# Kernel tuning notes

Measured on AMD Instinct MI355X. Metric: run time of the kernel, lower is better.

## Reference

```python
import jax, jax.numpy as jnp
import numpy as np

N_A, N_B = 50000, 10000
E = 300000
IN_F, HID, BEL_OUT, INC_OUT = 256, 256, 128, 128


def _gconv(x_src, W, b, src, dst, n_src, n_dst):
    """DGL GraphConv with norm='both': D_in^{-1/2} A D_out^{-1/2} X W + b, degs clamped to >=1."""
    ones = jnp.ones(src.shape[0], x_src.dtype)
    deg_out = jnp.maximum(jax.ops.segment_sum(ones, src, num_segments=n_src), 1.0)
    deg_in = jnp.maximum(jax.ops.segment_sum(ones, dst, num_segments=n_dst), 1.0)
    h = (x_src * jax.lax.rsqrt(deg_out)[:, None]) @ W        # [n_src, out]
    agg = jax.ops.segment_sum(h[src], dst, num_segments=n_dst)  # scatter-add messages
    return agg * jax.lax.rsqrt(deg_in)[:, None] + b


def setup_inputs() -> dict:
    key = jax.random.key(0)
    ks = jax.random.split(key, 12)
    s = 1.0 / np.sqrt(IN_F)
    sh = 1.0 / np.sqrt(HID)
    return {
        "x_a": jax.random.normal(ks[0], (N_A, IN_F), jnp.float32),
        "x_b": jax.random.normal(ks[1], (N_B, IN_F), jnp.float32),
        "W1_bel": jax.random.normal(ks[2], (IN_F, HID), jnp.float32) * s,
        "b1_bel": jnp.zeros((HID,), jnp.float32),
        "W1_inc": jax.random.normal(ks[3], (IN_F, HID), jnp.float32) * s,
        "b1_inc": jnp.zeros((HID,), jnp.float32),
        "W2_bel": jax.random.normal(ks[4], (HID, BEL_OUT), jnp.float32) * sh,
        "b2_bel": jnp.zeros((BEL_OUT,), jnp.float32),
        "W2_inc": jax.random.normal(ks[5], (HID, INC_OUT), jnp.float32) * sh,
        "b2_inc": jnp.zeros((INC_OUT,), jnp.float32),
        "bel_src": jax.random.randint(ks[6], (E,), 0, N_A, jnp.int32),
        "bel_dst": jax.random.randint(ks[7], (E,), 0, N_B, jnp.int32),
        "inc_src": jax.random.randint(ks[8], (E,), 0, N_B, jnp.int32),
        "inc_dst": jax.random.randint(ks[9], (E,), 0, N_A, jnp.int32),
    }


def reference(x_a, x_b, W1_bel, b1_bel, W1_inc, b1_inc, W2_bel, b2_bel,
              W2_inc, b2_inc, bel_src, bel_dst, inc_src, inc_dst):
    n_a, n_b = x_a.shape[0], x_b.shape[0]
    # layer 1 (HeteroGraphConv, mean over a single relation per dst type = identity)
    h_b = _gconv(x_a, W1_bel, b1_bel, bel_src, bel_dst, n_a, n_b)  # 'belongs_to': A->B
    h_a = _gconv(x_b, W1_inc, b1_inc, inc_src, inc_dst, n_b, n_a)  # 'including' : B->A
    h_a = jax.nn.relu(h_a)
    h_b = jax.nn.relu(h_b)
    # layer 2
    out_b = _gconv(h_a, W2_bel, b2_bel, bel_src, bel_dst, n_a, n_b)  # [N_B, bel_out]
    out_a = _gconv(h_b, W2_inc, b2_inc, inc_src, inc_dst, n_b, n_a)  # [N_A, inc_out]
    return out_a, out_b
```

## Files before the change

### kernel.cpp

```cpp
#include <hip/hip_runtime.h>


#define NA 50000
#define NB 10000
#define NE 300000
#define GB 625
#define HB 1172
#define PB 64
#define CB 300

typedef unsigned short u16;
typedef unsigned int u32;
typedef __attribute__((ext_vector_type(8))) short short8;
typedef __attribute__((ext_vector_type(4))) float f32x4;
typedef __attribute__((ext_vector_type(2))) float f32x2;
typedef __attribute__((ext_vector_type(4))) unsigned short u16x4;
typedef __attribute__((ext_vector_type(4))) int i32x4;

__device__ __forceinline__ int xcc_id(){
  return (int)(__builtin_amdgcn_s_getreg(63508) & 7u);
}

__device__ __forceinline__ float bf2f(u16 h){
  union { u32 u; float f; } x; x.u = ((u32)h) << 16; return x.f;
}
__device__ __forceinline__ u16 f2bf(float f){
  union { float f; u32 u; } x; x.f = f;
  u32 r = (x.u + 0x7FFFu + ((x.u >> 16) & 1u)) >> 16;
  return (u16)r;
}

__device__ __forceinline__ void pack_elem(int t,
    const float* __restrict__ W1b, const float* __restrict__ W1i,
    const float* __restrict__ W2b, const float* __restrict__ W2i,
    u16* __restrict__ pwh, u16* __restrict__ pwl){
  const float* W; int N; int tt;
  if (t < 65536)       { W = W1b; N = 256; tt = t; }
  else if (t < 131072) { W = W1i; N = 256; tt = t - 65536; }
  else if (t < 163840) { W = W2b; N = 128; tt = t - 131072; }
  else                 { W = W2i; N = 128; tt = t - 163840; }
  int j = tt & 7, lane = (tt >> 3) & 63, tile = tt >> 9;
  int nT = N >> 4;
  int nt = tile % nT, kt = tile / nT;
  int k = kt * 32 + ((lane >> 4) << 3) + j;
  int n = nt * 16 + (lane & 15);
  float v = W[k * N + n];
  u16 hi = f2bf(v);
  pwh[t] = hi;
  pwl[t] = f2bf(v - bf2f(hi));
}

__global__ __launch_bounds__(256) void pre_kernel(
    int* __restrict__ z, int nz4, const float* __restrict__ W1i,
    u16* __restrict__ pwh, u16* __restrict__ pwl){
  int g = blockIdx.x * blockDim.x + threadIdx.x;
  int s = gridDim.x * blockDim.x;
  i32x4* z4 = (i32x4*)z;
  i32x4 zero = {0, 0, 0, 0};
  for (int i = g; i < nz4; i += s) __builtin_nontemporal_store(zero, z4 + i);
  for (int t = g; t < 65536; t += s)
    pack_elem(65536 + t, nullptr, W1i, nullptr, nullptr, pwh, pwl);
}

__device__ __forceinline__ void gemm_dev(int blk, const float* __restrict__ A,
                                         const u16* __restrict__ PWH,
                                         const u16* __restrict__ PWL,
                                         const float* __restrict__ bias,
                                         const float* __restrict__ rs,
                                         float* __restrict__ Cf,
                                         u16* __restrict__ C16,
                                         int M, int nT, int wpsShift,
                                         int doRelu, int ldC, int colOff){
  int wave = blk * 4 + (threadIdx.x >> 6);
  int lane = threadIdx.x & 63;
  int strips = M >> 4;
  int strip = wave >> wpsShift;
  if (strip >= strips) return;
  int slice = wave & ((1 << wpsShift) - 1);
  int ntPer = nT >> wpsShift;
  int ntStart = slice * ntPer;
  int r16 = lane & 15, quad = lane >> 4;
  int m0 = strip << 4;
  const float* aBase = A + (size_t)(m0 + r16) * 256 + quad * 8;
  short8 ah[8], al[8];
#pragma unroll
  for (int kt = 0; kt < 8; ++kt){
    float4 p0 = *(const float4*)(aBase + kt * 32);
    float4 p1 = *(const float4*)(aBase + kt * 32 + 4);
    float v[8] = {p0.x, p0.y, p0.z, p0.w, p1.x, p1.y, p1.z, p1.w};
    short8 h, l;
#pragma unroll
    for (int j = 0; j < 8; ++j){
      u16 hb = f2bf(v[j]);
      h[j] = (short)hb;
      l[j] = (short)f2bf(v[j] - bf2f(hb));
    }
    ah[kt] = h; al[kt] = l;
  }
  float rscale[4];
#pragma unroll
  for (int r = 0; r < 4; ++r) rscale[r] = rs ? rs[m0 + quad * 4 + r] : 1.f;
  for (int nt = ntStart; nt < ntStart + ntPer; ++nt){
    f32x4 acc = {0.f, 0.f, 0.f, 0.f};
    const u16* bh = PWH + ((size_t)nt * 64 + lane) * 8;
    const u16* bl = PWL + ((size_t)nt * 64 + lane) * 8;
#pragma unroll
    for (int kt = 0; kt < 8; ++kt){
      short8 wh = *(const short8*)(bh + (size_t)kt * nT * 512);
      short8 wl = *(const short8*)(bl + (size_t)kt * nT * 512);
      acc = __builtin_amdgcn_mfma_f32_16x16x32_bf16(ah[kt], wh, acc, 0, 0, 0);
      acc = __builtin_amdgcn_mfma_f32_16x16x32_bf16(al[kt], wh, acc, 0, 0, 0);
      acc = __builtin_amdgcn_mfma_f32_16x16x32_bf16(ah[kt], wl, acc, 0, 0, 0);
    }
    int col = nt * 16 + r16;
    float bv = bias ? bias[col] : 0.f;
#pragma unroll
    for (int r = 0; r < 4; ++r){
      float v = acc[r] * rscale[r] + bv;
      if (doRelu) v = fmaxf(v, 0.f);
      size_t o = (size_t)(m0 + quad * 4 + r) * ldC + colOff + col;
      if (C16) __builtin_nontemporal_store(f2bf(v), C16 + o);
      else     __builtin_nontemporal_store(v, Cf + o);
    }
  }
}

__global__ __launch_bounds__(256) void mega_kernel(
    const float* __restrict__ xb,
    const u16* __restrict__ WH1i, const u16* __restrict__ WL1i,
    u16* __restrict__ G12,
    const int* __restrict__ bs, const int* __restrict__ bd,
    const int* __restrict__ isc, const int* __restrict__ idt,
    int* __restrict__ c_bs8, int* __restrict__ c_bd8,
    int* __restrict__ c_is8, int* __restrict__ c_id,
    int* __restrict__ rank_bel, int* __restrict__ rank_inc,
    const float* __restrict__ W1b, const float* __restrict__ W2b,
    const float* __restrict__ W2i,
    u16* __restrict__ pwh, u16* __restrict__ pwl,
    const float* __restrict__ xa, u16* __restrict__ xa16){
  int blk = blockIdx.x;
  if (blk < GB){
    gemm_dev(blk, xb, WH1i, WL1i, nullptr, nullptr,
             nullptr, G12, NB, 16, 2, 0, 384, 0);
  } else if (blk < GB + HB){
    int xcc = xcc_id();
    int g = (blk - GB) * blockDim.x + threadIdx.x;
    int s = HB * blockDim.x;
    for (int e = g; e < NE; e += s){
      __hip_atomic_fetch_add(&c_bs8[bs[e] * 8 + xcc], 1,
                             __ATOMIC_RELAXED, __HIP_MEMORY_SCOPE_WORKGROUP);
      int rb = __hip_atomic_fetch_add(&c_bd8[bd[e] * 8 + xcc], 1,
                             __ATOMIC_RELAXED, __HIP_MEMORY_SCOPE_WORKGROUP);
      rank_bel[e] = rb | (xcc << 27);
      __hip_atomic_fetch_add(&c_is8[isc[e] * 8 + xcc], 1,
                             __ATOMIC_RELAXED, __HIP_MEMORY_SCOPE_WORKGROUP);
      rank_inc[e] = atomicAdd(&c_id[idt[e]], 1);
    }
  } else if (blk < GB + HB + PB){
    int g = (blk - GB - HB) * blockDim.x + threadIdx.x;
    int s = PB * blockDim.x;
    for (int v = g; v < 131072; v += s){
      int t = v < 65536 ? v : v + 65536;
      pack_elem(t, W1b, nullptr, W2b, W2i, pwh, pwl);
    }
  } else {
    int g = ((blk - GB - HB - PB) * blockDim.x + threadIdx.x) * 4;
    int s = CB * blockDim.x * 4;
    for (int i = g; i < NA * 256; i += s){
      float4 v = *(const float4*)(xa + i);
      u16x4 o;
      o.x = f2bf(v.x); o.y = f2bf(v.y); o.z = f2bf(v.z); o.w = f2bf(v.w);
      __builtin_nontemporal_store(o, (u16x4*)(xa16 + i));
    }
  }
}

__global__ __launch_bounds__(1024) void scan_scales_kernel(
    const int* __restrict__ c_bs8, const int* __restrict__ c_bd8,
    const int* __restrict__ c_is8, const int* __restrict__ c_id,
    int* __restrict__ off_bel, int* __restrict__ off_inc,
    float* __restrict__ s_ob, float* __restrict__ s_ib,
    float* __restrict__ s_oi, float* __restrict__ s_ii){
  if (blockIdx.x >= 2){
    int g = (blockIdx.x - 2) * blockDim.x + threadIdx.x;
    int s = (gridDim.x - 2) * blockDim.x;
    for (int i = g; i < NA; i += s){
      i32x4 a0 = *(const i32x4*)(c_bs8 + i * 8);
      i32x4 a1 = *(const i32x4*)(c_bs8 + i * 8 + 4);
      int a = a0[0] + a0[1] + a0[2] + a0[3] + a1[0] + a1[1] + a1[2] + a1[3];
      s_ob[i] = rsqrtf((float)(a > 1 ? a : 1));
      int b = c_id[i]; s_ii[i] = rsqrtf((float)(b > 1 ? b : 1));
      if (i < NB){
        i32x4 c0 = *(const i32x4*)(c_bd8 + i * 8);
        i32x4 c1 = *(const i32x4*)(c_bd8 + i * 8 + 4);
        int c = c0[0] + c0[1] + c0[2] + c0[3] + c1[0] + c1[1] + c1[2] + c1[3];
        s_ib[i] = rsqrtf((float)(c > 1 ? c : 1));
        i32x4 d0 = *(const i32x4*)(c_is8 + i * 8);
        i32x4 d1 = *(const i32x4*)(c_is8 + i * 8 + 4);
        int d = d0[0] + d0[1] + d0[2] + d0[3] + d1[0] + d1[1] + d1[2] + d1[3];
        s_oi[i] = rsqrtf((float)(d > 1 ? d : 1));
      }
    }
    return;
  }
  __shared__ int wsum[16];
  int tid = threadIdx.x, lane = tid & 63, wid = tid >> 6;
  if (blockIdx.x == 0){
    const int SEG = 10;
    int i0 = tid * SEG;
    int v[SEG];
#pragma unroll
    for (int r = 0; r < SEG; ++r){
      int idx = i0 + r;
      int sv = 0;
      if (idx < NB){
        i32x4 q0 = *(const i32x4*)(c_bd8 + idx * 8);
        i32x4 q1 = *(const i32x4*)(c_bd8 + idx * 8 + 4);
        sv = q0[0] + q0[1] + q0[2] + q0[3] + q1[0] + q1[1] + q1[2] + q1[3];
      }
      v[r] = sv;
    }
    int sum = 0;
#pragma unroll
    for (int r = 0; r < SEG; ++r) sum += v[r];
    int x = sum;
#pragma unroll
    for (int d = 1; d < 64; d <<= 1){
      int t = __shfl_up(x, d, 64);
      if (lane >= d) x += t;
    }
    if (lane == 63) wsum[wid] = x;
    __syncthreads();
    if (wid == 0){
      int ws = (lane < 16) ? wsum[lane] : 0;
#pragma unroll
      for (int d = 1; d < 16; d <<= 1){
        int t = __shfl_up(ws, d, 64);
        if (lane >= d) ws += t;
      }
      if (lane < 16) wsum[lane] = ws;
    }
    __syncthreads();
    int run = (wid ? wsum[wid - 1] : 0) + (x - sum);
#pragma unroll
    for (int r = 0; r < SEG; ++r){
      int idx = i0 + r;
      if (idx < NB) off_bel[idx] = run;
      run += v[r];
    }
    if (tid == 0) off_bel[NB] = wsum[15];
  } else {
    const int n = NA;
    int seg = (n + 1023) >> 10;
    int i0 = tid * seg;
    int lim = i0 + seg; if (lim > n) lim = n;
    int sum = 0;
    for (int i = i0; i < lim; ++i) sum += c_id[i];
    int x = sum;
#pragma unroll
    for (int d = 1; d < 64; d <<= 1){
      int t = __shfl_up(x, d, 64);
      if (lane >= d) x += t;
    }
    if (lane == 63) wsum[wid] = x;
    __syncthreads();
    if (wid == 0){
      int ws = (lane < 16) ? wsum[lane] : 0;
#pragma unroll
      for (int d = 1; d < 16; d <<= 1){
        int t = __shfl_up(ws, d, 64);
        if (lane >= d) ws += t;
      }
      if (lane < 16) wsum[lane] = ws;
    }
    __syncthreads();
    int run = (wid ? wsum[wid - 1] : 0) + (x - sum);
    for (int i = i0; i < lim; ++i){ off_inc[i] = run; run += c_id[i]; }
    if (tid == 0) off_inc[n] = wsum[15];
  }
}

__global__ __launch_bounds__(256) void fill_kernel(
    const int* __restrict__ bs, const int* __restrict__ bd,
    const int* __restrict__ isc, const int* __restrict__ idt,
    const int* __restrict__ rank_bel, const int* __restrict__ rank_inc,
    const int* __restrict__ off_bel, const int* __restrict__ off_inc,
    const int* __restrict__ c_bd8,
    int* __restrict__ csr_bel, int* __restrict__ csr_inc){
  int g = blockIdx.x * blockDim.x + threadIdx.x;
  int s = gridDim.x * blockDim.x;
  for (int e = g; e < NE; e += s){
    int pb = rank_bel[e];
    int xcc = pb >> 27;
    int rb = pb & ((1 << 27) - 1);
    int d = bd[e];
    i32x4 q0 = *(const i32x4*)(c_bd8 + d * 8);
    i32x4 q1 = *(const i32x4*)(c_bd8 + d * 8 + 4);
    int p = 0;
    p += (xcc > 0) ? q0[0] : 0;
    p += (xcc > 1) ? q0[1] : 0;
    p += (xcc > 2) ? q0[2] : 0;
    p += (xcc > 3) ? q0[3] : 0;
    p += (xcc > 4) ? q1[0] : 0;
    p += (xcc > 5) ? q1[1] : 0;
    p += (xcc > 6) ? q1[2] : 0;
    csr_bel[off_bel[d] + p + rb] = bs[e];
    csr_inc[off_inc[idt[e]] + rank_inc[e]] = isc[e];
  }
}

__global__ __launch_bounds__(256) void agg_bel_kernel(
    const u16* __restrict__ X, const float* __restrict__ ss,
    const int* __restrict__ off, const int* __restrict__ csr,
    float* __restrict__ Pf, int nDst){
  int wave = blockIdx.x * 4 + (threadIdx.x >> 6);
  int lane = threadIdx.x & 63;
  if (wave >= nDst) return;
  int b0 = off[wave], b1 = off[wave + 1];
  int deg = b1 - b0;
  int part = lane >> 5;
  int cl = lane & 31;
  int c = cl * 8;
  float acc[8];
#pragma unroll
  for (int q = 0; q < 8; ++q) acc[q] = 0.f;
  int idx = 0; float sc = 0.f;
  if (lane < deg){
    idx = csr[b0 + lane];
    sc = ss ? ss[idx] : 1.f;
  }
  int lim = deg < 64 ? deg : 64;
  for (int u = 0; u < lim; u += 8){
    const u16* addr[4]; float w[4];
#pragma unroll
    for (int k = 0; k < 4; ++k){
      int e = u + k * 2 + part;
      int t = e < lim ? e : 0;
      int s0 = __shfl(idx, t, 64);
      float c0 = __shfl(sc, t, 64);
      w[k] = e < lim ? c0 : 0.f;
      addr[k] = X + (size_t)s0 * 256 + c;
    }
    short8 v[4];
#pragma unroll
    for (int k = 0; k < 4; ++k) v[k] = *(const short8*)addr[k];
#pragma unroll
    for (int k = 0; k < 4; ++k)
#pragma unroll
      for (int q = 0; q < 8; ++q) acc[q] += bf2f((u16)v[k][q]) * w[k];
  }
  for (int j = b0 + 64 + part; j < b1; j += 2){
    int s0 = csr[j];
    float c0 = ss ? ss[s0] : 1.f;
    short8 v0 = *(const short8*)(X + (size_t)s0 * 256 + c);
#pragma unroll
    for (int q = 0; q < 8; ++q) acc[q] += bf2f((u16)v0[q]) * c0;
  }
#pragma unroll
  for (int q = 0; q < 8; ++q) acc[q] += __shfl_xor(acc[q], 32, 64);
  if (part == 0){
    f32x4 f0 = {acc[0], acc[1], acc[2], acc[3]};
    f32x4 f1 = {acc[4], acc[5], acc[6], acc[7]};
    __builtin_nontemporal_store(f0, (f32x4*)(Pf + (size_t)wave * 256 + c));
    __builtin_nontemporal_store(f1, (f32x4*)(Pf + (size_t)wave * 256 + c + 4));
  }
}

__global__ __launch_bounds__(256) void gemmHG_kernel(
    const float* __restrict__ Pb,
    const u16* __restrict__ WH1b, const u16* __restrict__ WL1b,
    const float* __restrict__ b1b, const float* __restrict__ s_ib,
    const u16* __restrict__ WH2i, const u16* __restrict__ WL2i,
    u16* __restrict__ G12){
  __shared__ float Hs[16][260];
  int w = threadIdx.x >> 6;
  int lane = threadIdx.x & 63;
  int r16 = lane & 15, quad = lane >> 4;
  int m0 = blockIdx.x << 4;
  const float* aBase = Pb + (size_t)(m0 + r16) * 256 + quad * 8;
  short8 ah[8], al[8];
#pragma unroll
  for (int kt = 0; kt < 8; ++kt){
    float4 p0 = *(const float4*)(aBase + kt * 32);
    float4 p1 = *(const float4*)(aBase + kt * 32 + 4);
    float v[8] = {p0.x, p0.y, p0.z, p0.w, p1.x, p1.y, p1.z, p1.w};
    short8 h, l;
#pragma unroll
    for (int j = 0; j < 8; ++j){
      u16 hb = f2bf(v[j]);
      h[j] = (short)hb;
      l[j] = (short)f2bf(v[j] - bf2f(hb));
    }
    ah[kt] = h; al[kt] = l;
  }
  float rs1[4];
#pragma unroll
  for (int r = 0; r < 4; ++r) rs1[r] = s_ib[m0 + quad * 4 + r];
  for (int nt = w * 4; nt < w * 4 + 4; ++nt){
    f32x4 acc = {0.f, 0.f, 0.f, 0.f};
    const u16* bh = WH1b + ((size_t)nt * 64 + lane) * 8;
    const u16* bl = WL1b + ((size_t)nt * 64 + lane) * 8;
#pragma unroll
    for (int kt = 0; kt < 8; ++kt){
      short8 wh = *(const short8*)(bh + (size_t)kt * 16 * 512);
      short8 wl = *(const short8*)(bl + (size_t)kt * 16 * 512);
      acc = __builtin_amdgcn_mfma_f32_16x16x32_bf16(ah[kt], wh, acc, 0, 0, 0);
      acc = __builtin_amdgcn_mfma_f32_16x16x32_bf16(al[kt], wh, acc, 0, 0, 0);
      acc = __builtin_amdgcn_mfma_f32_16x16x32_bf16(ah[kt], wl, acc, 0, 0, 0);
    }
    int col = nt * 16 + r16;
    float bv = b1b[col];
#pragma unroll
    for (int r = 0; r < 4; ++r)
      Hs[quad * 4 + r][col] = fmaxf(acc[r] * rs1[r] + bv, 0.f);
  }
  __syncthreads();
  short8 ah2[8], al2[8];
#pragma unroll
  for (int kt = 0; kt < 8; ++kt){
    float4 p0 = *(const float4*)&Hs[r16][kt * 32 + quad * 8];
    float4 p1 = *(const float4*)&Hs[r16][kt * 32 + quad * 8 + 4];
    float v[8] = {p0.x, p0.y, p0.z, p0.w, p1.x, p1.y, p1.z, p1.w};
    short8 h, l;
#pragma unroll
    for (int j = 0; j < 8; ++j){
      u16 hb = f2bf(v[j]);
      h[j] = (short)hb;
      l[j] = (short)f2bf(v[j] - bf2f(hb));
    }
    ah2[kt] = h; al2[kt] = l;
  }
  for (int nt = w * 2; nt < w * 2 + 2; ++nt){
    f32x4 acc = {0.f, 0.f, 0.f, 0.f};
    const u16* bh = WH2i + ((size_t)nt * 64 + lane) * 8;
    const u16* bl = WL2i + ((size_t)nt * 64 + lane) * 8;
#pragma unroll
    for (int kt = 0; kt < 8; ++kt){
      short8 wh = *(const short8*)(bh + (size_t)kt * 8 * 512);
      short8 wl = *(const short8*)(bl + (size_t)kt * 8 * 512);
      acc = __builtin_amdgcn_mfma_f32_16x16x32_bf16(ah2[kt], wh, acc, 0, 0, 0);
      acc = __builtin_amdgcn_mfma_f32_16x16x32_bf16(al2[kt], wh, acc, 0, 0, 0);
      acc = __builtin_amdgcn_mfma_f32_16x16x32_bf16(ah2[kt], wl, acc, 0, 0, 0);
    }
    int col = nt * 16 + r16;
#pragma unroll
    for (int r = 0; r < 4; ++r){
      u16 o = f2bf(acc[r]);
      __builtin_nontemporal_store(o, G12 + (size_t)(m0 + quad * 4 + r) * 384 + 256 + col);
    }
  }
}

__global__ __launch_bounds__(256) void agg_inc2_kernel(
    const u16* __restrict__ G12, const int* __restrict__ off,
    const int* __restrict__ csr, const float* __restrict__ s_oi,
    const float* __restrict__ s_ii, const float* __restrict__ s_ob,
    const float* __restrict__ b1i, const float* __restrict__ b2i,
    u16* __restrict__ Ha, float* __restrict__ outa){
  int wave = blockIdx.x * 4 + (threadIdx.x >> 6);
  int lane = threadIdx.x & 63;
  if (wave >= NA) return;
  int b0 = off[wave], b1 = off[wave + 1];
  int deg = b1 - b0;
  int c1 = lane * 4;
  int c2 = lane * 2;
  float acc[6];
#pragma unroll
  for (int q = 0; q < 6; ++q) acc[q] = 0.f;
  int idx = 0; float sc = 0.f;
  if (lane < deg){
    idx = csr[b0 + lane];
    sc = s_oi[idx];
  }
  int lim = deg < 64 ? deg : 64;
  for (int u = 0; u < lim; u += 4){
    ushort4 va[4]; ushort2 vb[4]; float w[4];
#pragma unroll
    for (int k = 0; k < 4; ++k){
      int e = u + k;
      int t = e < lim ? e : 0;
      int se = __shfl(idx, t, 64);
      float c0 = __shfl(sc, t, 64);
      w[k] = e < lim ? c0 : 0.f;
      const u16* r = G12 + (size_t)se * 384;
      va[k] = *(const ushort4*)(r + c1);
      vb[k] = *(const ushort2*)(r + 256 + c2);
    }
#pragma unroll
    for (int k = 0; k < 4; ++k){
      acc[0] += bf2f(va[k].x) * w[k];
      acc[1] += bf2f(va[k].y) * w[k];
      acc[2] += bf2f(va[k].z) * w[k];
      acc[3] += bf2f(va[k].w) * w[k];
      acc[4] += bf2f(vb[k].x) * w[k];
      acc[5] += bf2f(vb[k].y) * w[k];
    }
  }
  for (int j = b0 + 64; j < b1; ++j){
    int se = csr[j];
    float c0 = s_oi[se];
    const u16* r = G12 + (size_t)se * 384;
    ushort4 va = *(const ushort4*)(r + c1);
    ushort2 vb = *(const ushort2*)(r + 256 + c2);
    acc[0] += bf2f(va.x) * c0; acc[1] += bf2f(va.y) * c0;
    acc[2] += bf2f(va.z) * c0; acc[3] += bf2f(va.w) * c0;
    acc[4] += bf2f(vb.x) * c0; acc[5] += bf2f(vb.y) * c0;
  }
  float sii = s_ii[wave], sob = s_ob[wave];
  float4 bb1 = *(const float4*)(b1i + c1);
  f32x2 bb2 = *(const f32x2*)(b2i + c2);
  u16x4 o1;
  o1.x = f2bf(fmaxf(acc[0] * sii + bb1.x, 0.f) * sob);
  o1.y = f2bf(fmaxf(acc[1] * sii + bb1.y, 0.f) * sob);
  o1.z = f2bf(fmaxf(acc[2] * sii + bb1.z, 0.f) * sob);
  o1.w = f2bf(fmaxf(acc[3] * sii + bb1.w, 0.f) * sob);
  __builtin_nontemporal_store(o1, (u16x4*)(Ha + (size_t)wave * 256 + c1));
  f32x2 o2 = {acc[4] * sii + bb2.x, acc[5] * sii + bb2.y};
  __builtin_nontemporal_store(o2, (f32x2*)(outa + (size_t)wave * 128 + c2));
}

__global__ __launch_bounds__(256) void gemm_kernel(
    const float* __restrict__ A,
    const u16* __restrict__ PWH, const u16* __restrict__ PWL,
    const float* __restrict__ bias, const float* __restrict__ rs,
    float* __restrict__ Cf, u16* __restrict__ C16,
    int M, int nT, int wpsShift, int doRelu, int ldC, int colOff){
  gemm_dev(blockIdx.x, A, PWH, PWL, bias, rs, Cf, C16,
           M, nT, wpsShift, doRelu, ldC, colOff);
}

extern "C" void kernel_launch(void* const* d_in, const int* in_sizes, int n_in,
                              void* d_out, int out_size, void* d_ws, size_t ws_size,
                              hipStream_t stream){
  const float* x_a = (const float*)d_in[0];
  const float* x_b = (const float*)d_in[1];
  const float* W1b = (const float*)d_in[2];
  const float* b1b = (const float*)d_in[3];
  const float* W1i = (const float*)d_in[4];
  const float* b1i = (const float*)d_in[5];
  const float* W2b = (const float*)d_in[6];
  const float* b2b = (const float*)d_in[7];
  const float* W2i = (const float*)d_in[8];
  const float* b2i = (const float*)d_in[9];
  const int* bs  = (const int*)d_in[10];
  const int* bd  = (const int*)d_in[11];
  const int* isc = (const int*)d_in[12];
  const int* idt = (const int*)d_in[13];

  char* w = (char*)d_ws;
  size_t o = 0;
  auto take = [&](size_t bytes) -> void* {
    void* p = w + o; o = (o + bytes + 255) & ~(size_t)255; return p;
  };
  int* zint = (int*)take((size_t)610000 * sizeof(int));
  int* c_bs8 = zint;
  int* c_bd8 = zint + 400000;
  int* c_is8 = zint + 480000;
  int* c_id  = zint + 560000;
  int* rank_bel = (int*)take(NE * sizeof(int));
  int* rank_inc = (int*)take(NE * sizeof(int));
  int* off_bel = (int*)take((NB + 1) * sizeof(int));
  int* off_inc = (int*)take((NA + 1) * sizeof(int));
  int* csr_bel = (int*)take(NE * sizeof(int));
  int* csr_inc = (int*)take(NE * sizeof(int));
  float* s_ob = (float*)take(NA * sizeof(float));
  float* s_ib = (float*)take(NB * sizeof(float));
  float* s_oi = (float*)take(NB * sizeof(float));
  float* s_ii = (float*)take(NA * sizeof(float));
  u16* pwh = (u16*)take(196608 * sizeof(u16));
  u16* pwl = (u16*)take(196608 * sizeof(u16));
  u16* pwh1b = pwh, *pwh1i = pwh + 65536, *pwh2b = pwh + 131072, *pwh2i = pwh + 163840;
  u16* pwl1b = pwl, *pwl1i = pwl + 65536, *pwl2b = pwl + 131072, *pwl2i = pwl + 163840;
  u16* xa16 = (u16*)take((size_t)NA * 256 * sizeof(u16));
  u16* G12  = (u16*)take((size_t)NB * 384 * sizeof(u16));
  u16* H_a  = (u16*)take((size_t)NA * 256 * sizeof(u16));
  float* P_b = (float*)take((size_t)NB * 256 * sizeof(float));

  float* out_a = (float*)d_out;
  float* out_b = (float*)d_out + (size_t)NA * 128;

  pre_kernel<<<256, 256, 0, stream>>>(zint, 610000 / 4, W1i, pwh, pwl);
  mega_kernel<<<GB + HB + PB + CB, 256, 0, stream>>>(
      x_b, pwh1i, pwl1i, G12,
      bs, bd, isc, idt, c_bs8, c_bd8, c_is8, c_id, rank_bel, rank_inc,
      W1b, W2b, W2i, pwh, pwl, x_a, xa16);
  scan_scales_kernel<<<52, 1024, 0, stream>>>(c_bs8, c_bd8, c_is8, c_id,
                                              off_bel, off_inc,
                                              s_ob, s_ib, s_oi, s_ii);
  fill_kernel<<<1172, 256, 0, stream>>>(bs, bd, isc, idt, rank_bel, rank_inc,
                                        off_bel, off_inc, c_bd8,
                                        csr_bel, csr_inc);
  agg_bel_kernel<<<2500, 256, 0, stream>>>(xa16, s_ob, off_bel, csr_bel, P_b, NB);
  gemmHG_kernel<<<625, 256, 0, stream>>>(P_b, pwh1b, pwl1b, b1b, s_ib,
                                         pwh2i, pwl2i, G12);
  agg_inc2_kernel<<<12500, 256, 0, stream>>>(G12, off_inc, csr_inc, s_oi,
                                             s_ii, s_ob, b1i, b2i, H_a, out_a);
  agg_bel_kernel<<<2500, 256, 0, stream>>>(H_a, nullptr, off_bel, csr_bel, P_b, NB);
  gemm_kernel<<<625, 256, 0, stream>>>(P_b, pwh2b, pwl2b, b2b, s_ib,
                                       out_b, nullptr, NB, 8, 2, 0, 128, 0);
}
```

Baseline: 395.2 us.

## Compute source out-degrees via LDS-privatized packed 16-bit histograms per edge slice

Out-degree counts for bel_src and inc_src are now built in pre_kernel, with LDS histograms per edge slice using packed 16-bit counters. Slice partials are written to global memory and reduced in scan_scales_kernel. Destination counters drop the per-XCC 8-way replication and go back to plain global atomics, which simplifies fill_kernel's CSR placement. The aim is to remove two global atomic streams from mega_kernel and shrink the zeroed workspace, at the cost of 64-way partial reductions per node and more contention on the single destination counters.

```diff
diff --git a/kernel.cpp b/kernel.cpp
--- a/kernel.cpp
+++ b/kernel.cpp
@@ -8,6 +8,10 @@
 #define HB 1172
 #define PB 64
 #define CB 300
+#define NSL 64
+#define EPS 4688
+#define NWBS 12500
+#define NWIS 5000
 
 typedef unsigned short u16;
 typedef unsigned int u32;
@@ -16,10 +20,6 @@
 typedef __attribute__((ext_vector_type(2))) float f32x2;
 typedef __attribute__((ext_vector_type(4))) unsigned short u16x4;
 typedef __attribute__((ext_vector_type(4))) int i32x4;
-
-__device__ __forceinline__ int xcc_id(){
-  return (int)(__builtin_amdgcn_s_getreg(63508) & 7u);
-}
 
 __device__ __forceinline__ float bf2f(u16 h){
   union { u32 u; float f; } x; x.u = ((u32)h) << 16; return x.f;
@@ -51,15 +51,46 @@
 }
 
 __global__ __launch_bounds__(256) void pre_kernel(
-    int* __restrict__ z, int nz4, const float* __restrict__ W1i,
+    const int* __restrict__ bs, const int* __restrict__ isc,
+    u32* __restrict__ pbs, u32* __restrict__ pis,
+    int* __restrict__ zint, int nz, const float* __restrict__ W1i,
     u16* __restrict__ pwh, u16* __restrict__ pwl){
-  int g = blockIdx.x * blockDim.x + threadIdx.x;
-  int s = gridDim.x * blockDim.x;
-  i32x4* z4 = (i32x4*)z;
-  i32x4 zero = {0, 0, 0, 0};
-  for (int i = g; i < nz4; i += s) __builtin_nontemporal_store(zero, z4 + i);
-  for (int t = g; t < 65536; t += s)
-    pack_elem(65536 + t, nullptr, W1i, nullptr, nullptr, pwh, pwl);
+  __shared__ u32 lh[NWBS];
+  int blk = blockIdx.x, tid = threadIdx.x;
+  if (blk < 192){
+    int isB = blk >= 128;
+    int slice = isB ? (blk - 128) : (blk & 63);
+    int range = isB ? 0 : (blk >> 6);
+    int nw = isB ? NWIS : NWBS;
+    int lo = range * 25000;
+    int nbins = isB ? NB : 25000;
+    const int* src = isB ? isc : bs;
+    u32* dst = isB ? (pis + (size_t)slice * NWIS)
+                   : (pbs + (size_t)blk * NWBS);
+    for (int i = tid; i < nw; i += 256) lh[i] = 0;
+    __syncthreads();
+    int e0 = slice * EPS;
+    int e1 = e0 + EPS; if (e1 > NE) e1 = NE;
+    const i32x4* s4 = (const i32x4*)src;
+    for (int i = e0 / 4 + tid; i < e1 / 4; i += 256){
+      i32x4 v = s4[i];
+#pragma unroll
+      for (int k = 0; k < 4; ++k){
+        int b = v[k] - lo;
+        if ((unsigned)b < (unsigned)nbins)
+          atomicAdd(&lh[b >> 1], 1u << ((b & 1) << 4));
+      }
+    }
+    __syncthreads();
+    for (int i = tid; i < nw; i += 256)
+      __builtin_nontemporal_store(lh[i], dst + i);
+  } else {
+    int g = (blk - 192) * 256 + tid;
+    int s = 128 * 256;
+    for (int i = g; i < nz; i += s) zint[i] = 0;
+    for (int t = g; t < 65536; t += s)
+      pack_elem(65536 + t, nullptr, W1i, nullptr, nullptr, pwh, pwl);
+  }
 }
 
 __device__ __forceinline__ void gemm_dev(int blk, const float* __restrict__ A,
@@ -129,10 +160,8 @@
     const float* __restrict__ xb,
     const u16* __restrict__ WH1i, const u16* __restrict__ WL1i,
     u16* __restrict__ G12,
-    const int* __restrict__ bs, const int* __restrict__ bd,
-    const int* __restrict__ isc, const int* __restrict__ idt,
-    int* __restrict__ c_bs8, int* __restrict__ c_bd8,
-    int* __restrict__ c_is8, int* __restrict__ c_id,
+    const int* __restrict__ bd, const int* __restrict__ idt,
+    int* __restrict__ c_bd, int* __restrict__ c_id,
     int* __restrict__ rank_bel, int* __restrict__ rank_inc,
     const float* __restrict__ W1b, const float* __restrict__ W2b,
     const float* __restrict__ W2i,
@@ -143,17 +172,10 @@
     gemm_dev(blk, xb, WH1i, WL1i, nullptr, nullptr,
              nullptr, G12, NB, 16, 2, 0, 384, 0);
   } else if (blk < GB + HB){
-    int xcc = xcc_id();
     int g = (blk - GB) * blockDim.x + threadIdx.x;
     int s = HB * blockDim.x;
     for (int e = g; e < NE; e += s){
-      __hip_atomic_fetch_add(&c_bs8[bs[e] * 8 + xcc], 1,
-                             __ATOMIC_RELAXED, __HIP_MEMORY_SCOPE_WORKGROUP);
-      int rb = __hip_atomic_fetch_add(&c_bd8[bd[e] * 8 + xcc], 1,
-                             __ATOMIC_RELAXED, __HIP_MEMORY_SCOPE_WORKGROUP);
-      rank_bel[e] = rb | (xcc << 27);
-      __hip_atomic_fetch_add(&c_is8[isc[e] * 8 + xcc], 1,
-                             __ATOMIC_RELAXED, __HIP_MEMORY_SCOPE_WORKGROUP);
+      rank_bel[e] = atomicAdd(&c_bd[bd[e]], 1);
       rank_inc[e] = atomicAdd(&c_id[idt[e]], 1);
     }
   } else if (blk < GB + HB + PB){
@@ -176,8 +198,8 @@
 }
 
 __global__ __launch_bounds__(1024) void scan_scales_kernel(
-    const int* __restrict__ c_bs8, const int* __restrict__ c_bd8,
-    const int* __restrict__ c_is8, const int* __restrict__ c_id,
+    const u32* __restrict__ pbs, const u32* __restrict__ pis,
+    const int* __restrict__ c_bd, const int* __restrict__ c_id,
     int* __restrict__ off_bel, int* __restrict__ off_inc,
     float* __restrict__ s_ob, float* __restrict__ s_ib,
     float* __restrict__ s_oi, float* __restrict__ s_ii){
@@ -185,20 +207,24 @@
     int g = (blockIdx.x - 2) * blockDim.x + threadIdx.x;
     int s = (gridDim.x - 2) * blockDim.x;
     for (int i = g; i < NA; i += s){
-      i32x4 a0 = *(const i32x4*)(c_bs8 + i * 8);
-      i32x4 a1 = *(const i32x4*)(c_bs8 + i * 8 + 4);
-      int a = a0[0] + a0[1] + a0[2] + a0[3] + a1[0] + a1[1] + a1[2] + a1[3];
+      int range = (i >= 25000);
+      int loc = i - range * 25000;
+      int word = loc >> 1, sh = (loc & 1) << 4;
+      const u32* base = pbs + (size_t)(range << 6) * NWBS + word;
+      int a = 0;
+#pragma unroll 8
+      for (int b = 0; b < NSL; ++b)
+        a += (int)((base[(size_t)b * NWBS] >> sh) & 0xFFFFu);
       s_ob[i] = rsqrtf((float)(a > 1 ? a : 1));
-      int b = c_id[i]; s_ii[i] = rsqrtf((float)(b > 1 ? b : 1));
+      int d = c_id[i]; s_ii[i] = rsqrtf((float)(d > 1 ? d : 1));
       if (i < NB){
-        i32x4 c0 = *(const i32x4*)(c_bd8 + i * 8);
-        i32x4 c1 = *(const i32x4*)(c_bd8 + i * 8 + 4);
-        int c = c0[0] + c0[1] + c0[2] + c0[3] + c1[0] + c1[1] + c1[2] + c1[3];
-        s_ib[i] = rsqrtf((float)(c > 1 ? c : 1));
-        i32x4 d0 = *(const i32x4*)(c_is8 + i * 8);
-        i32x4 d1 = *(const i32x4*)(c_is8 + i * 8 + 4);
-        int d = d0[0] + d0[1] + d0[2] + d0[3] + d1[0] + d1[1] + d1[2] + d1[3];
-        s_oi[i] = rsqrtf((float)(d > 1 ? d : 1));
+        int c = c_bd[i]; s_ib[i] = rsqrtf((float)(c > 1 ? c : 1));
+        int word2 = i >> 1, sh2 = (i & 1) << 4;
+        int e2 = 0;
+#pragma unroll 8
+        for (int b = 0; b < NSL; ++b)
+          e2 += (int)((pis[(size_t)b * NWIS + word2] >> sh2) & 0xFFFFu);
+        s_oi[i] = rsqrtf((float)(e2 > 1 ? e2 : 1));
       }
     }
     return;
@@ -212,13 +238,7 @@
 #pragma unroll
     for (int r = 0; r < SEG; ++r){
       int idx = i0 + r;
-      int sv = 0;
-      if (idx < NB){
-        i32x4 q0 = *(const i32x4*)(c_bd8 + idx * 8);
-        i32x4 q1 = *(const i32x4*)(c_bd8 + idx * 8 + 4);
-        sv = q0[0] + q0[1] + q0[2] + q0[3] + q1[0] + q1[1] + q1[2] + q1[3];
-      }
-      v[r] = sv;
+      v[r] = (idx < NB) ? c_bd[idx] : 0;
     }
     int sum = 0;
 #pragma unroll
@@ -285,26 +305,11 @@
     const int* __restrict__ isc, const int* __restrict__ idt,
     const int* __restrict__ rank_bel, const int* __restrict__ rank_inc,
     const int* __restrict__ off_bel, const int* __restrict__ off_inc,
-    const int* __restrict__ c_bd8,
     int* __restrict__ csr_bel, int* __restrict__ csr_inc){
   int g = blockIdx.x * blockDim.x + threadIdx.x;
   int s = gridDim.x * blockDim.x;
   for (int e = g; e < NE; e += s){
-    int pb = rank_bel[e];
-    int xcc = pb >> 27;
-    int rb = pb & ((1 << 27) - 1);
-    int d = bd[e];
-    i32x4 q0 = *(const i32x4*)(c_bd8 + d * 8);
-    i32x4 q1 = *(const i32x4*)(c_bd8 + d * 8 + 4);
-    int p = 0;
-    p += (xcc > 0) ? q0[0] : 0;
-    p += (xcc > 1) ? q0[1] : 0;
-    p += (xcc > 2) ? q0[2] : 0;
-    p += (xcc > 3) ? q0[3] : 0;
-    p += (xcc > 4) ? q1[0] : 0;
-    p += (xcc > 5) ? q1[1] : 0;
-    p += (xcc > 6) ? q1[2] : 0;
-    csr_bel[off_bel[d] + p + rb] = bs[e];
+    csr_bel[off_bel[bd[e]] + rank_bel[e]] = bs[e];
     csr_inc[off_inc[idt[e]] + rank_inc[e]] = isc[e];
   }
 }
@@ -552,11 +557,11 @@
   auto take = [&](size_t bytes) -> void* {
     void* p = w + o; o = (o + bytes + 255) & ~(size_t)255; return p;
   };
-  int* zint = (int*)take((size_t)610000 * sizeof(int));
-  int* c_bs8 = zint;
-  int* c_bd8 = zint + 400000;
-  int* c_is8 = zint + 480000;
-  int* c_id  = zint + 560000;
+  int* zint = (int*)take(60000 * sizeof(int));
+  int* c_bd = zint;
+  int* c_id = zint + 10000;
+  u32* pbs = (u32*)take((size_t)128 * NWBS * sizeof(u32));
+  u32* pis = (u32*)take((size_t)NSL * NWIS * sizeof(u32));
   int* rank_bel = (int*)take(NE * sizeof(int));
   int* rank_inc = (int*)take(NE * sizeof(int));
   int* off_bel = (int*)take((NB + 1) * sizeof(int));
@@ -579,17 +584,17 @@
   float* out_a = (float*)d_out;
   float* out_b = (float*)d_out + (size_t)NA * 128;
 
-  pre_kernel<<<256, 256, 0, stream>>>(zint, 610000 / 4, W1i, pwh, pwl);
+  pre_kernel<<<320, 256, 0, stream>>>(bs, isc, pbs, pis,
+                                      zint, 60000, W1i, pwh, pwl);
   mega_kernel<<<GB + HB + PB + CB, 256, 0, stream>>>(
       x_b, pwh1i, pwl1i, G12,
-      bs, bd, isc, idt, c_bs8, c_bd8, c_is8, c_id, rank_bel, rank_inc,
+      bd, idt, c_bd, c_id, rank_bel, rank_inc,
       W1b, W2b, W2i, pwh, pwl, x_a, xa16);
-  scan_scales_kernel<<<52, 1024, 0, stream>>>(c_bs8, c_bd8, c_is8, c_id,
+  scan_scales_kernel<<<52, 1024, 0, stream>>>(pbs, pis, c_bd, c_id,
                                               off_bel, off_inc,
                                               s_ob, s_ib, s_oi, s_ii);
   fill_kernel<<<1172, 256, 0, stream>>>(bs, bd, isc, idt, rank_bel, rank_inc,
-                                        off_bel, off_inc, c_bd8,
-                                        csr_bel, csr_inc);
+                                        off_bel, off_inc, csr_bel, csr_inc);
   agg_bel_kernel<<<2500, 256, 0, stream>>>(xa16, s_ob, off_bel, csr_bel, P_b, NB);
   gemmHG_kernel<<<625, 256, 0, stream>>>(P_b, pwh1b, pwl1b, b1b, s_ib,
                                          pwh2i, pwl2i, G12);
```

New measurement: 381.0 us. 1.04x faster.
